# Kernel tuning notes

Hardware: AMD Instinct MI355X
Metric: run time of the kernel (lower is better)

Reference implementation:

```python
import jax, jax.numpy as jnp
import numpy as np

B, T, D = 16, 512, 256
HH = D // 2   # per-direction hidden of bidirectional GRU
G, Z, R, NA = 32, 8, 16, 18


def _gru_step(h, x, wih, whh, bih, bhh):
    # torch.nn.GRUCell math
    gi = x @ wih.T + bih
    gh = h @ whh.T + bhh
    ir, iz, inn = jnp.split(gi, 3, axis=-1)
    hr, hz, hn = jnp.split(gh, 3, axis=-1)
    r = jax.nn.sigmoid(ir + hr)
    z = jax.nn.sigmoid(iz + hz)
    n = jnp.tanh(inn + r * hn)
    return (1.0 - z) * n + z * h


def _gru_seq(x_tbd, wih, whh, bih, bhh):
    h0 = jnp.zeros((x_tbd.shape[1], whh.shape[1]), x_tbd.dtype)
    def step(h, x):
        h = _gru_step(h, x, wih, whh, bih, bhh)
        return h, h
    _, hs = jax.lax.scan(step, h0, x_tbd)
    return hs  # (T, B, H)


def setup_inputs() -> dict:
    key = jax.random.key(0)
    ks = jax.random.split(key, 26)
    rn = lambda k, s, sc: jax.random.normal(k, s, jnp.float32) * sc
    d = {
        'e_seq': rn(ks[0], (B, T, D), 1.0),
        'eps':   rn(ks[1], (B, T, Z), 1.0),
        # acausal bidirectional GRU (fwd + bwd cells)
        'wih_f': rn(ks[2], (3 * HH, D), D ** -0.5),  'whh_f': rn(ks[3], (3 * HH, HH), HH ** -0.5),
        'bih_f': jnp.zeros((3 * HH,)), 'bhh_f': jnp.zeros((3 * HH,)),
        'wih_b': rn(ks[4], (3 * HH, D), D ** -0.5),  'whh_b': rn(ks[5], (3 * HH, HH), HH ** -0.5),
        'bih_b': jnp.zeros((3 * HH,)), 'bhh_b': jnp.zeros((3 * HH,)),
        # controller encoder GRUCell(2D -> G) + heads
        'wih_e': rn(ks[6], (3 * G, 2 * D), (2 * D) ** -0.5), 'whh_e': rn(ks[7], (3 * G, G), G ** -0.5),
        'bih_e': jnp.zeros((3 * G,)), 'bhh_e': jnp.zeros((3 * G,)),
        'mu_w': rn(ks[8], (Z, G), G ** -0.5),  'mu_b': jnp.zeros((Z,)),
        'lv_w': rn(ks[9], (Z, G), G ** -0.5),  'lv_b': jnp.zeros((Z,)),
        # switching unit MLP (D+G+Z -> 64 -> 1)
        'sw1_w': rn(ks[10], (64, D + G + Z), (D + G + Z) ** -0.5), 'sw1_b': jnp.zeros((64,)),
        'sw2_w': rn(ks[11], (1, 64), 64 ** -0.5), 'sw2_b': jnp.zeros((1,)),
        # decoder hypernet (Z -> 32 -> 2*D*R)
        'dec1_w': rn(ks[12], (32, Z), Z ** -0.5), 'dec1_b': jnp.zeros((32,)),
        'dec2_w': rn(ks[13], (2 * D * R, 32), 32 ** -0.5), 'dec2_b': jnp.zeros((2 * D * R,)),
        # final norm + action head
        'ln_g': jnp.ones((D,)), 'ln_b': jnp.zeros((D,)),
        'head_w': rn(ks[14], (NA, D), D ** -0.5), 'head_b': jnp.zeros((NA,)),
    }
    return d


def _forward(e_seq, eps, wih_f, whh_f, bih_f, bhh_f, wih_b, whh_b, bih_b, bhh_b,
             wih_e, whh_e, bih_e, bhh_e, mu_w, mu_b, lv_w, lv_b,
             sw1_w, sw1_b, sw2_w, sw2_b, dec1_w, dec1_b, dec2_w, dec2_b,
             ln_g, ln_b, head_w, head_b):
    Bz, Tt, Dm = e_seq.shape
    e_tbd = jnp.swapaxes(e_seq, 0, 1)                      # (T, B, D)
    # AcausalEmbedder: bidirectional GRU
    fwd = _gru_seq(e_tbd, wih_f, whh_f, bih_f, bhh_f)
    bwd = _gru_seq(e_tbd[::-1], wih_b, whh_b, bih_b, bhh_b)[::-1]
    s_tbd = jnp.concatenate([fwd, bwd], axis=-1)           # (T, B, D)
    eps_tbd = jnp.swapaxes(eps, 0, 1)

    h0 = jnp.zeros((Bz, whh_e.shape[1]), e_seq.dtype)
    z0 = jnp.zeros((Bz, mu_w.shape[0]), e_seq.dtype)

    def step(carry, xs):
        h, z_prev = carry
        e_t, s_t, eps_t = xs
        h = _gru_step(h, jnp.concatenate([e_t, s_t], axis=-1), wih_e, whh_e, bih_e, bhh_e)
        mu = h @ mu_w.T + mu_b
        logvar = h @ lv_w.T + lv_b
        # switching unit uses updated h (causal)
        hid = jnp.tanh(jnp.concatenate([e_t, h, z_prev], axis=-1) @ sw1_w.T + sw1_b)
        beta = jax.nn.sigmoid(hid @ sw2_w.T + sw2_b)       # (B, 1)
        z = beta * (mu + jnp.exp(0.5 * logvar) * eps_t) + (1.0 - beta) * z_prev
        return (h, jax.lax.stop_gradient(z)), (mu, logvar, beta, z)

    _, (mu_t, lv_t, be_t, z_t) = jax.lax.scan(step, (h0, z0), (e_tbd, s_tbd, eps_tbd))
    mu_seq = jnp.swapaxes(mu_t, 0, 1)
    logvar_seq = jnp.swapaxes(lv_t, 0, 1)
    beta_seq = jnp.swapaxes(be_t, 0, 1)
    z_seq = jnp.swapaxes(z_t, 0, 1)                        # (B, T, Z)

    # ControllerDecoder: z -> (A, Bm); apply U = A @ Bm^T without materializing U
    hmid = jnp.tanh(z_seq @ dec1_w.T + dec1_b)
    ab = hmid @ dec2_w.T + dec2_b                          # (B, T, 2*D*R)
    DR = ab.shape[-1] // 2
    A = ab[..., :DR].reshape(Bz, Tt, Dm, -1)               # (B, T, D, R)
    Bm = ab[..., DR:].reshape(Bz, Tt, Dm, -1)
    tmp = jnp.einsum('btdr,btd->btr', Bm, e_seq)
    perturbed = e_seq + jnp.einsum('btdr,btr->btd', A, tmp)

    # final LayerNorm + action head on obs positions
    mean = perturbed.mean(-1, keepdims=True)
    var = perturbed.var(-1, keepdims=True)
    xn = (perturbed - mean) * jax.lax.rsqrt(var + 1e-5) * ln_g + ln_b
    logits = xn @ head_w.T + head_b                        # (B, T, NA)
    return logits, mu_seq, logvar_seq, beta_seq, z_seq


def reference(e_seq, eps, wih_f, whh_f, bih_f, bhh_f, wih_b, whh_b, bih_b, bhh_b,
              wih_e, whh_e, bih_e, bhh_e, mu_w, mu_b, lv_w, lv_b,
              sw1_w, sw1_b, sw2_w, sw2_b, dec1_w, dec1_b, dec2_w, dec2_b,
              ln_g, ln_b, head_w, head_b):
    return _forward(e_seq, eps, wih_f, whh_f, bih_f, bhh_f, wih_b, whh_b, bih_b, bhh_b,
                    wih_e, whh_e, bih_e, bhh_e, mu_w, mu_b, lv_w, lv_b,
                    sw1_w, sw1_b, sw2_w, sw2_b, dec1_w, dec1_b, dec2_w, dec2_b,
                    ln_g, ln_b, head_w, head_b)
```

## Files before the change

kernel.cpp:

```cpp
#include <hip/hip_runtime.h>

#define TT 512
#define BB 16
#define DD 256
#define HHH 128
#define GG 32
#define ZZ 8
#define RR_ 16
#define NAA 18

typedef _Float16 h2v __attribute__((ext_vector_type(2)));
typedef __attribute__((ext_vector_type(4))) float f4;
typedef __attribute__((ext_vector_type(4))) int i4;

__device__ __forceinline__ float sigmoid_(float x) { return 1.f / (1.f + __expf(-x)); }
__device__ __forceinline__ float tanh_(float x) { float e = __expf(2.f * x); return 1.f - 2.f / (e + 1.f); }
__device__ __forceinline__ float dot4(float4 a, float4 b) {
    return a.x * b.x + a.y * b.y + a.z * b.z + a.w * b.w;
}
__device__ __forceinline__ h2v u2h2(unsigned u) { union { unsigned u; h2v h; } c; c.u = u; return c.h; }

__device__ __forceinline__ void lds_barrier() {
    asm volatile("s_waitcnt lgkmcnt(0)" ::: "memory");
    __builtin_amdgcn_s_barrier();
}

template <int CTRL, int RM, int BM, bool BC>
__device__ __forceinline__ float dpp_add_f(float v) {
    return v + __int_as_float(__builtin_amdgcn_update_dpp(0, __float_as_int(v), CTRL, RM, BM, BC));
}
__device__ __forceinline__ float wave_sum_bcast(float p) {
    p = dpp_add_f<0x111, 0xf, 0xf, true>(p);
    p = dpp_add_f<0x112, 0xf, 0xf, true>(p);
    p = dpp_add_f<0x114, 0xf, 0xf, true>(p);
    p = dpp_add_f<0x118, 0xf, 0xf, true>(p);
    p = dpp_add_f<0x142, 0xa, 0xf, false>(p);
    p = dpp_add_f<0x143, 0xc, 0xf, false>(p);
    return __int_as_float(__builtin_amdgcn_readlane(__float_as_int(p), 63));
}
__device__ __forceinline__ float quad_sum(float v) {
    v = dpp_add_f<0xB1, 0xf, 0xf, true>(v);
    v = dpp_add_f<0x4E, 0xf, 0xf, true>(v);
    return v;
}
__device__ __forceinline__ float rdlane(float v, int l) {
    return __int_as_float(__builtin_amdgcn_readlane(__float_as_int(v), l));
}

__global__ __launch_bounds__(256) void pack_w(
    const float* __restrict__ wf, const float* __restrict__ wb,
    const float* __restrict__ we,
    unsigned* __restrict__ pk, unsigned* __restrict__ pk_e)
{
    int i = blockIdx.x * 256 + threadIdx.x;
    if (i < 49152) {
        int dir = i / 24576; int r = i % 24576;
        int w = r / 3072;    int r2 = r % 3072;
        int T = r2 / 1024;   int r3 = r2 % 1024;
        int kt = r3 / 256;   int r4 = r3 % 256;
        int lane = r4 / 4;   int jd = r4 % 4;
        const float* wsrc = dir ? wb : wf;
        int row = T * 128 + 16 * w + (lane & 15);
        int k0 = kt * 32 + (lane >> 4) * 8 + 2 * jd;
        union { _Float16 h[2]; unsigned u; } c;
        c.h[0] = (_Float16)wsrc[row * 128 + k0];
        c.h[1] = (_Float16)wsrc[row * 128 + k0 + 1];
        pk[i] = c.u;
    } else if (i < 50688) {
        int ie = i - 49152;
        int s = ie / 384;  int rem = ie % 384;
        int k = rem / 12;  int e = rem % 12;
        int j = e / 4;     int m = e % 4;
        int row = j * 32 + k, k0 = 8 * s + 2 * m;
        union { _Float16 h[2]; unsigned u; } c;
        c.h[0] = (_Float16)we[row * 32 + k0];
        c.h[1] = (_Float16)we[row * 32 + k0 + 1];
        pk_e[ie] = c.u;
    }
}

__global__ __launch_bounds__(256) void gemm_k(
    const float* __restrict__ A, int K, const float* __restrict__ W, int ldw,
    const float* __restrict__ bias, float* __restrict__ Out, int ldout, int N, int accFlag)
{
    __shared__ float At[64][36];
    __shared__ float Wt[32][36];
    int row0 = blockIdx.x * 64, n0 = blockIdx.y * 32;
    int tid = threadIdx.x;
    int tx = tid & 15, ty = tid >> 4;
    float acc[4][2] = {};
    for (int k0 = 0; k0 < K; k0 += 32) {
        #pragma unroll
        for (int i = 0; i < 8; ++i) {
            int idx = tid + i * 256; int rr = idx >> 5, kk = idx & 31;
            At[rr][kk] = A[(size_t)(row0 + rr) * K + k0 + kk];
        }
        #pragma unroll
        for (int i = 0; i < 4; ++i) {
            int idx = tid + i * 256; int nn = idx >> 5, kk = idx & 31;
            Wt[nn][kk] = (n0 + nn < N) ? W[(size_t)(n0 + nn) * ldw + k0 + kk] : 0.f;
        }
        __syncthreads();
        #pragma unroll
        for (int kk = 0; kk < 32; kk += 4) {
            float4 w0 = *(const float4*)&Wt[tx][kk];
            float4 w1 = *(const float4*)&Wt[tx + 16][kk];
            #pragma unroll
            for (int rr = 0; rr < 4; ++rr) {
                float4 av = *(const float4*)&At[ty * 4 + rr][kk];
                acc[rr][0] += dot4(av, w0);
                acc[rr][1] += dot4(av, w1);
            }
        }
        __syncthreads();
    }
    #pragma unroll
    for (int cc = 0; cc < 2; ++cc) {
        int n = n0 + tx + cc * 16;
        if (n < N) {
            float badd = bias ? bias[n] : 0.f;
            #pragma unroll
            for (int rr = 0; rr < 4; ++rr) {
                int row = row0 + ty * 4 + rr;
                float v = acc[rr][cc] + badd;
                if (accFlag) Out[(size_t)row * ldout + n] += v;
                else         Out[(size_t)row * ldout + n] = v;
            }
        }
    }
}

__global__ __launch_bounds__(256) void gemm_gi(
    const float* __restrict__ A,
    const float* __restrict__ wf, const float* __restrict__ bf, float* __restrict__ of,
    const float* __restrict__ wb, const float* __restrict__ bb, float* __restrict__ ob)
{
    __shared__ float At[64][36];
    __shared__ float Wt[32][36];
    int y = blockIdx.y;
    const float* W; const float* bias; float* Out; int n0;
    if (y < 12) { W = wf; bias = bf; Out = of; n0 = y * 32; }
    else        { W = wb; bias = bb; Out = ob; n0 = (y - 12) * 32; }
    int row0 = blockIdx.x * 64;
    int tid = threadIdx.x;
    int tx = tid & 15, ty = tid >> 4;
    float acc[4][2] = {};
    for (int k0 = 0; k0 < 256; k0 += 32) {
        #pragma unroll
        for (int i = 0; i < 8; ++i) {
            int idx = tid + i * 256; int rr = idx >> 5, kk = idx & 31;
            At[rr][kk] = A[(size_t)(row0 + rr) * 256 + k0 + kk];
        }
        #pragma unroll
        for (int i = 0; i < 4; ++i) {
            int idx = tid + i * 256; int nn = idx >> 5, kk = idx & 31;
            Wt[nn][kk] = W[(size_t)(n0 + nn) * 256 + k0 + kk];
        }
        __syncthreads();
        #pragma unroll
        for (int kk = 0; kk < 32; kk += 4) {
            float4 w0 = *(const float4*)&Wt[tx][kk];
            float4 w1 = *(const float4*)&Wt[tx + 16][kk];
            #pragma unroll
            for (int rr = 0; rr < 4; ++rr) {
                float4 av = *(const float4*)&At[ty * 4 + rr][kk];
                acc[rr][0] += dot4(av, w0);
                acc[rr][1] += dot4(av, w1);
            }
        }
        __syncthreads();
    }
    #pragma unroll
    for (int cc = 0; cc < 2; ++cc) {
        int n = n0 + tx + cc * 16;
        float badd = bias[n];
        #pragma unroll
        for (int rr = 0; rr < 4; ++rr) {
            int row = row0 + ty * 4 + rr;
            Out[(size_t)row * 384 + n] = acc[rr][cc] + badd;
        }
    }
}

struct __align__(16) SmGru { _Float16 hb[2][128]; };
struct __align__(16) SmGemm { float At[64][36]; float Wt[32][36]; };
union __align__(16) SmU { SmGru g; SmGemm m; };

__device__ __forceinline__ void gemm_tile256(
    const float* __restrict__ A, int K, const float* __restrict__ W, int ldw,
    const float* __restrict__ bias, float* __restrict__ Out, int ldout, int N,
    int row0, int n0, SmGemm& sm)
{
    int tid = threadIdx.x;
    int tx = tid & 15, ty = tid >> 4;
    float acc[4][2] = {};
    for (int k0 = 0; k0 < K; k0 += 32) {
        #pragma unroll
        for (int i = 0; i < 8; ++i) {
            int idx = tid + i * 256; int rr = idx >> 5, kk = idx & 31;
            sm.At[rr][kk] = A[(size_t)(row0 + rr) * K + k0 + kk];
        }
        #pragma unroll
        for (int i = 0; i < 4; ++i) {
            int idx = tid + i * 256; int nn = idx >> 5, kk = idx & 31;
            sm.Wt[nn][kk] = (n0 + nn < N) ? W[(size_t)(n0 + nn) * ldw + k0 + kk] : 0.f;
        }
        __syncthreads();
        #pragma unroll
        for (int kk = 0; kk < 32; kk += 4) {
            float4 w0 = *(const float4*)&sm.Wt[tx][kk];
            float4 w1 = *(const float4*)&sm.Wt[tx + 16][kk];
            #pragma unroll
            for (int rr = 0; rr < 4; ++rr) {
                float4 av = *(const float4*)&sm.At[ty * 4 + rr][kk];
                acc[rr][0] += dot4(av, w0);
                acc[rr][1] += dot4(av, w1);
            }
        }
        __syncthreads();
    }
    #pragma unroll
    for (int cc = 0; cc < 2; ++cc) {
        int n = n0 + tx + cc * 16;
        if (n < N) {
            float badd = bias[n];
            #pragma unroll
            for (int rr = 0; rr < 4; ++rr)
                Out[(size_t)(row0 + ty * 4 + rr) * ldout + n] = acc[rr][cc] + badd;
        }
    }
}

__global__ __launch_bounds__(256, 2) void gru_fused(
    const float* __restrict__ gi_f, const float* __restrict__ gi_b,
    const unsigned* __restrict__ pk,
    const float* __restrict__ bhh_f, const float* __restrict__ bhh_b,
    float* __restrict__ s_seq,
    const float* __restrict__ e,
    const float* __restrict__ wih_e, const float* __restrict__ bih_e, float* __restrict__ gie,
    const float* __restrict__ sw1_w, const float* __restrict__ sw1_b, float* __restrict__ swe)
{
    __shared__ SmU sm;
    int bx = blockIdx.x;
    if (bx >= 416) {
        int t = bx - 416;
        gemm_tile256(e, 256, sw1_w, 296, sw1_b, swe, 64, 64, (t & 127) * 64, (t >> 7) * 32, sm.m);
        return;
    }
    if (bx >= 32) {
        int t = bx - 32;
        gemm_tile256(e, 256, wih_e, 512, bih_e, gie, 96, 96, (t & 127) * 64, (t >> 7) * 32, sm.m);
        return;
    }

    int dir = bx >> 4, b = bx & 15;
    const float* gi  = dir ? gi_b  : gi_f;
    const float* bhh = dir ? bhh_b : bhh_f;
    int tid = threadIdx.x;
    int w = tid >> 6;
    int lane = tid & 63;
    int quad = lane >> 4;
    int j = 32 * w + (lane & 31);

    i4 bf[2][3][4];
    #pragma unroll
    for (int tt = 0; tt < 2; ++tt)
        #pragma unroll
        for (int T = 0; T < 3; ++T)
            #pragma unroll
            for (int kt = 0; kt < 4; ++kt)
                bf[tt][T][kt] = *(const i4*)(pk + (size_t)((((dir * 8 + 2 * w + tt) * 3 + T) * 4 + kt) * 64 + lane) * 4);
    #pragma unroll
    for (int tt = 0; tt < 2; ++tt)
        #pragma unroll
        for (int T = 0; T < 3; ++T)
            #pragma unroll
            for (int kt = 0; kt < 4; ++kt)
                asm volatile("" : "+a"(bf[tt][T][kt]));

    if (tid < 128) sm.g.hb[0][tid] = (_Float16)0.f;

    float bhr = 0.f, bhz = 0.f, bhn = 0.f;
    float gra = 0.f, gza = 0.f, gna = 0.f;
    float grb = 0.f, gzb = 0.f, gnb = 0.f;
    float hreg = 0.f;
    if (lane < 32) {
        bhr = bhh[j]; bhz = bhh[128 + j]; bhn = bhh[256 + j];
        int t0 = dir ? 511 : 0;
        int t1 = dir ? 510 : 1;
        size_t p0 = (size_t)(b * TT + t0) * 384;
        size_t p1 = (size_t)(b * TT + t1) * 384;
        gra = gi[p0 + j]; gza = gi[p0 + 128 + j]; gna = gi[p0 + 256 + j];
        grb = gi[p1 + j]; gzb = gi[p1 + 128 + j]; gnb = gi[p1 + 256 + j];
    }
    __syncthreads();

    int cur = 0;
    auto body = [&](int step, float& gr, float& gz, float& gn) {
        i4 af[4];
        #pragma unroll
        for (int kt = 0; kt < 4; ++kt)
            af[kt] = *(const i4*)(&sm.g.hb[cur][kt * 32 + quad * 8]);
        f4 accr0 = {0.f, 0.f, 0.f, 0.f}, accr1 = {0.f, 0.f, 0.f, 0.f};
        f4 accz0 = {0.f, 0.f, 0.f, 0.f}, accz1 = {0.f, 0.f, 0.f, 0.f};
        f4 accn0 = {0.f, 0.f, 0.f, 0.f}, accn1 = {0.f, 0.f, 0.f, 0.f};
        asm volatile("s_nop 3" : "+v"(accr0), "+v"(accz0), "+v"(accn0),
                                 "+v"(accr1), "+v"(accz1), "+v"(accn1));
        #pragma unroll
        for (int kt = 0; kt < 4; ++kt) {
            asm volatile("v_mfma_f32_16x16x32_f16 %0, %1, %2, %0" : "+v"(accr0) : "v"(af[kt]), "a"(bf[0][0][kt]));
            asm volatile("v_mfma_f32_16x16x32_f16 %0, %1, %2, %0" : "+v"(accz0) : "v"(af[kt]), "a"(bf[0][1][kt]));
            asm volatile("v_mfma_f32_16x16x32_f16 %0, %1, %2, %0" : "+v"(accn0) : "v"(af[kt]), "a"(bf[0][2][kt]));
            asm volatile("v_mfma_f32_16x16x32_f16 %0, %1, %2, %0" : "+v"(accr1) : "v"(af[kt]), "a"(bf[1][0][kt]));
            asm volatile("v_mfma_f32_16x16x32_f16 %0, %1, %2, %0" : "+v"(accz1) : "v"(af[kt]), "a"(bf[1][1][kt]));
            asm volatile("v_mfma_f32_16x16x32_f16 %0, %1, %2, %0" : "+v"(accn1) : "v"(af[kt]), "a"(bf[1][2][kt]));
        }
        asm volatile("s_nop 7\n\ts_nop 7" : "+v"(accr0), "+v"(accz0), "+v"(accn0),
                                            "+v"(accr1), "+v"(accz1), "+v"(accn1));
        if (lane < 32) {
            int t = dir ? (511 - step) : step;
            int p = b * TT + t;
            bool hi = lane >= 16;
            float ar = hi ? accr1[0] : accr0[0];
            float az = hi ? accz1[0] : accz0[0];
            float an = hi ? accn1[0] : accn0[0];
            float r = sigmoid_(gr + bhr + ar);
            float z = sigmoid_(gz + bhz + az);
            float n = tanh_(gn + r * (bhn + an));
            float hn = (1.f - z) * n + z * hreg;
            hreg = hn;
            sm.g.hb[cur ^ 1][j] = (_Float16)hn;
            s_seq[(size_t)p * 256 + dir * 128 + j] = hn;
            int s2 = step + 2;
            int tp = (s2 < 512) ? (dir ? (511 - s2) : s2) : t;
            size_t p2 = (size_t)(b * TT + tp) * 384;
            gr = gi[p2 + j]; gz = gi[p2 + 128 + j]; gn = gi[p2 + 256 + j];
        }
        lds_barrier();
        cur ^= 1;
    };

    for (int step = 0; step < 512; step += 2) {
        body(step,     gra, gza, gna);
        body(step + 1, grb, gzb, gnb);
    }
}

__global__ __launch_bounds__(128, 1) void ctrl_fused(
    const float* __restrict__ gie, const unsigned* __restrict__ pk_e,
    const float* __restrict__ bhh_e,
    const float* __restrict__ mu_w, const float* __restrict__ mu_b,
    const float* __restrict__ lv_w, const float* __restrict__ lv_b,
    const float* __restrict__ sw1_w, const float* __restrict__ sw2_w,
    const float* __restrict__ sw2_b,
    const float* __restrict__ swe,
    const float* __restrict__ eps,
    float* __restrict__ out_mu, float* __restrict__ out_lv,
    float* __restrict__ beta_o, float* __restrict__ z_o)
{
    int b = blockIdx.x;
    int tid = threadIdx.x;
    int wid = tid >> 6;
    int lane = tid & 63;
    int pbase = b * TT;

    __shared__ __align__(16) _Float16 hb[32][32];
    __shared__ __align__(16) float    hf[32][32];

    int k = lane >> 1, s2 = lane & 1;
    unsigned wg[24];
    float bhr = 0.f, bhz = 0.f, bhn = 0.f, hreg = 0.f;
    float g1[16] = {}, g2[16] = {}, g3[16] = {};
    if (wid == 0) {
        #pragma unroll
        for (int ss = 0; ss < 2; ++ss) {
            const uint4* wp = (const uint4*)(pk_e + ((size_t)((2 * s2 + ss) * 32) + k) * 12);
            #pragma unroll
            for (int i = 0; i < 3; ++i) {
                uint4 u = wp[i];
                wg[12 * ss + 4 * i + 0] = u.x;
                wg[12 * ss + 4 * i + 1] = u.y;
                wg[12 * ss + 4 * i + 2] = u.z;
                wg[12 * ss + 4 * i + 3] = u.w;
            }
        }
        if (lane < 32) hb[31][lane] = (_Float16)0.f;
        if (s2 == 0) {
            bhr = bhh_e[k]; bhz = bhh_e[32 + k]; bhn = bhh_e[64 + k];
            #pragma unroll
            for (int i = 0; i < 16; ++i) {
                size_t p = (size_t)(pbase + i) * 96;
                g1[i] = gie[p + k]; g2[i] = gie[p + 32 + k]; g3[i] = gie[p + 64 + k];
            }
        }
    }

    int x = lane >> 3, kind = (lane >> 2) & 1, s = lane & 3;
    float4 swh4[8];
    float4 wz0v = {0,0,0,0}, wz1v = {0,0,0,0}, mlw0 = {0,0,0,0}, mlw1 = {0,0,0,0};
    float w2 = 0.f, sb2 = 0.f, mlb = 0.f;
    float4 zr0 = {0.f, 0.f, 0.f, 0.f}, zr1 = {0.f, 0.f, 0.f, 0.f};
    float hp[16] = {}, ep[16] = {};
    if (wid == 1) {
        #pragma unroll
        for (int i = 0; i < 8; ++i)
            swh4[i] = *(const float4*)(sw1_w + (size_t)lane * 296 + 256 + 4 * i);
        wz0v = *(const float4*)(sw1_w + (size_t)lane * 296 + 288);
        wz1v = *(const float4*)(sw1_w + (size_t)lane * 296 + 292);
        w2 = sw2_w[lane];
        sb2 = sw2_b[0];
        const float* mw = kind ? lv_w : mu_w;
        mlw0 = *(const float4*)(mw + x * 32 + 8 * s);
        mlw1 = *(const float4*)(mw + x * 32 + 8 * s + 4);
        mlb = kind ? lv_b[x] : mu_b[x];
        #pragma unroll
        for (int i = 0; i < 16; ++i) {
            hp[i] = swe[(size_t)(pbase + i) * 64 + lane];
            ep[i] = eps[(size_t)(pbase + i) * 8 + x];
        }
    }
    __syncthreads();

    auto prod_step = [&](int t, float& ga, float& gb, float& gc) {
        const uint4* hv = (const uint4*)(&hb[(t - 1) & 31][16 * s2]);
        uint4 hA = hv[0], hB = hv[1];
        unsigned hw[8] = {hA.x, hA.y, hA.z, hA.w, hB.x, hB.y, hB.z, hB.w};
        float a0 = 0.f, a1 = 0.f, a2 = 0.f, c0 = 0.f, c1 = 0.f, c2 = 0.f;
        #pragma unroll
        for (int m = 0; m < 4; ++m) {
            a0 = __builtin_amdgcn_fdot2(u2h2(wg[m]),      u2h2(hw[m]),     a0, false);
            a1 = __builtin_amdgcn_fdot2(u2h2(wg[4 + m]),  u2h2(hw[m]),     a1, false);
            a2 = __builtin_amdgcn_fdot2(u2h2(wg[8 + m]),  u2h2(hw[m]),     a2, false);
            c0 = __builtin_amdgcn_fdot2(u2h2(wg[12 + m]), u2h2(hw[4 + m]), c0, false);
            c1 = __builtin_amdgcn_fdot2(u2h2(wg[16 + m]), u2h2(hw[4 + m]), c1, false);
            c2 = __builtin_amdgcn_fdot2(u2h2(wg[20 + m]), u2h2(hw[4 + m]), c2, false);
        }
        a0 += c0; a1 += c1; a2 += c2;
        a0 = dpp_add_f<0xB1, 0xf, 0xf, true>(a0);
        a1 = dpp_add_f<0xB1, 0xf, 0xf, true>(a1);
        a2 = dpp_add_f<0xB1, 0xf, 0xf, true>(a2);
        if (s2 == 0) {
            float r = sigmoid_(ga + bhr + a0);
            float z = sigmoid_(gb + bhz + a1);
            float n = tanh_(gc + r * (bhn + a2));
            float hn = (1.f - z) * n + z * hreg;
            hreg = hn;
            hb[t & 31][k] = (_Float16)hn;
            hf[t & 31][k] = hn;
            int t16 = (t + 16 < 512) ? (t + 16) : t;
            size_t p2 = (size_t)(pbase + t16) * 96;
            ga = gie[p2 + k]; gb = gie[p2 + 32 + k]; gc = gie[p2 + 64 + k];
        }
    };

    auto cons_step = [&](int t, float& hpi, float& epi) {
        int sl = t & 31;
        const float4* hv4 = (const float4*)(&hf[sl][0]);
        float4 h0 = hv4[0], h1 = hv4[1], h2 = hv4[2], h3 = hv4[3];
        float4 h4 = hv4[4], h5 = hv4[5], h6 = hv4[6], h7 = hv4[7];
        float d0 = dot4(swh4[0], h0) + dot4(swh4[1], h1);
        float d1 = dot4(swh4[2], h2) + dot4(swh4[3], h3);
        float d2 = dot4(swh4[4], h4) + dot4(swh4[5], h5);
        float d3 = dot4(swh4[6], h6) + dot4(swh4[7], h7);
        float hsum = (d0 + d1) + (d2 + d3);
        float4 hs0 = *(const float4*)(&hf[sl][8 * s]);
        float4 hs1 = *(const float4*)(&hf[sl][8 * s + 4]);
        float pacc = quad_sum(dot4(mlw0, hs0) + dot4(mlw1, hs1));
        float v = pacc + mlb;
        float other = __int_as_float(__builtin_amdgcn_ds_swizzle(__float_as_int(v), 0x101F));
        float muv = kind ? other : v;
        float lvv = kind ? v : other;
        float cand = muv + __expf(0.5f * lvv) * epi;
        float sc0 = rdlane(cand, 0),  sc1 = rdlane(cand, 8);
        float sc2 = rdlane(cand, 16), sc3 = rdlane(cand, 24);
        float sc4 = rdlane(cand, 32), sc5 = rdlane(cand, 40);
        float sc6 = rdlane(cand, 48), sc7 = rdlane(cand, 56);
        float az = dot4(wz0v, zr0) + dot4(wz1v, zr1);
        float a = (hpi + hsum) + az;
        float hid = tanh_(a);
        float beta = sigmoid_(wave_sum_bcast(w2 * hid) + sb2);
        float omb = 1.f - beta;
        zr0.x = beta * sc0 + omb * zr0.x; zr0.y = beta * sc1 + omb * zr0.y;
        zr0.z = beta * sc2 + omb * zr0.z; zr0.w = beta * sc3 + omb * zr0.w;
        zr1.x = beta * sc4 + omb * zr1.x; zr1.y = beta * sc5 + omb * zr1.y;
        zr1.z = beta * sc6 + omb * zr1.z; zr1.w = beta * sc7 + omb * zr1.w;
        int p = pbase + t;
        if (lane == 0) {
            beta_o[p] = beta;
            *(float4*)(z_o + (size_t)p * 8)     = zr0;
            *(float4*)(z_o + (size_t)p * 8 + 4) = zr1;
        }
        if ((lane & 7) == 0) out_mu[(size_t)p * 8 + x] = muv;
        if ((lane & 7) == 4) out_lv[(size_t)p * 8 + x] = lvv;
        int t16 = (t + 16 < 512) ? (t + 16) : t;
        hpi = swe[(size_t)(pbase + t16) * 64 + lane];
        epi = eps[(size_t)(pbase + t16) * 8 + x];
    };

    for (int ph = 0; ph < 33; ++ph) {
        if (wid == 0) {
            if (ph < 32) {
                int t0 = ph * 16;
                #pragma unroll
                for (int i = 0; i < 16; ++i)
                    prod_step(t0 + i, g1[i], g2[i], g3[i]);
            }
        } else {
            if (ph >= 1) {
                int t0 = (ph - 1) * 16;
                #pragma unroll
                for (int i = 0; i < 16; ++i)
                    cons_step(t0 + i, hp[i], ep[i]);
            }
        }
        lds_barrier();
    }
}

__global__ __launch_bounds__(256, 3) void decoder_final(
    const float* __restrict__ e_seq, const float* __restrict__ z_o,
    const float* __restrict__ dec1_w, const float* __restrict__ dec1_b,
    const float* __restrict__ dec2_w, const float* __restrict__ dec2_b,
    const float* __restrict__ ln_g, const float* __restrict__ ln_b,
    const float* __restrict__ head_w, const float* __restrict__ head_b,
    float* __restrict__ logits)
{
    __shared__ __align__(16) float e_l[8][256];
    __shared__ __align__(16) float hmid[8][32];
    __shared__ float zl[8][8];
    __shared__ float tmpw[8][16];
    __shared__ __align__(16) float partb[2048];
    __shared__ float red1[8][16];
    __shared__ float red2[8][16];
    __shared__ float stats[8][2];
    int tid = threadIdx.x;
    int p0 = blockIdx.x * 8;

    {
        const float4* eg = (const float4*)(e_seq + (size_t)p0 * 256);
        float4* el4 = (float4*)&e_l[0][0];
        el4[tid] = eg[tid];
        el4[tid + 256] = eg[tid + 256];
        if (tid < 64) ((float*)zl)[tid] = z_o[p0 * 8 + tid];
    }
    __syncthreads();
    {
        int pp = tid >> 5, g = tid & 31;
        float a = dec1_b[g];
        #pragma unroll
        for (int x = 0; x < 8; ++x) a += dec1_w[g * 8 + x] * zl[pp][x];
        hmid[pp][g] = tanh_(a);
    }
    __syncthreads();
    {
        int r = tid & 15, dgrp = tid >> 4;
        float acc[8];
        #pragma unroll
        for (int pp = 0; pp < 8; ++pp) acc[pp] = 0.f;
        for (int iblk = 0; iblk < 8; ++iblk) {
            float4 wr[2][8]; float wb[2]; int dd[2];
            #pragma unroll
            for (int ii = 0; ii < 2; ++ii) {
                int d = dgrp + 16 * (iblk * 2 + ii);
                dd[ii] = d;
                int row = 4096 + d * 16 + r;
                const float4* wp = (const float4*)(dec2_w + (size_t)row * 32);
                #pragma unroll
                for (int g = 0; g < 8; ++g) wr[ii][g] = wp[g];
                wb[ii] = dec2_b[row];
            }
            #pragma unroll 1
            for (int pp = 0; pp < 8; ++pp) {
                const float4* hv = (const float4*)hmid[pp];
                float b0 = wb[0], b1 = wb[1];
                #pragma unroll
                for (int g = 0; g < 8; ++g) {
                    float4 hh = hv[g];
                    b0 += dot4(wr[0][g], hh);
                    b1 += dot4(wr[1][g], hh);
                }
                acc[pp] += b0 * e_l[pp][dd[0]] + b1 * e_l[pp][dd[1]];
            }
        }
        #pragma unroll
        for (int pp = 0; pp < 8; ++pp) partb[(pp * 16 + r) * 16 + dgrp] = acc[pp];
    }
    __syncthreads();
    if (tid < 128) {
        int pp = tid >> 4, rr = tid & 15;
        float s = 0.f;
        #pragma unroll
        for (int dg = 0; dg < 16; ++dg) s += partb[(pp * 16 + rr) * 16 + dg];
        tmpw[pp][rr] = s;
    }
    __syncthreads();
    {
        int d = tid;
        float po[8];
        #pragma unroll
        for (int pp = 0; pp < 8; ++pp) po[pp] = e_l[pp][d];
        for (int rblk = 0; rblk < 8; ++rblk) {
            float4 wr[2][8]; float wb[2];
            #pragma unroll
            for (int ii = 0; ii < 2; ++ii) {
                int row = d * 16 + rblk * 2 + ii;
                const float4* wp = (const float4*)(dec2_w + (size_t)row * 32);
                #pragma unroll
                for (int g = 0; g < 8; ++g) wr[ii][g] = wp[g];
                wb[ii] = dec2_b[row];
            }
            #pragma unroll 1
            for (int pp = 0; pp < 8; ++pp) {
                const float4* hv = (const float4*)hmid[pp];
                float a0 = wb[0], a1 = wb[1];
                #pragma unroll
                for (int g = 0; g < 8; ++g) {
                    float4 hh = hv[g];
                    a0 += dot4(wr[0][g], hh);
                    a1 += dot4(wr[1][g], hh);
                }
                po[pp] += a0 * tmpw[pp][rblk * 2] + a1 * tmpw[pp][rblk * 2 + 1];
            }
        }
        #pragma unroll
        for (int pp = 0; pp < 8; ++pp) partb[pp * 256 + d] = po[pp];
    }
    __syncthreads();
    if (tid < 128) {
        int pp = tid >> 4, c = tid & 15;
        float s = 0.f, s2 = 0.f;
        #pragma unroll
        for (int i = 0; i < 16; ++i) { float v = partb[pp * 256 + c * 16 + i]; s += v; s2 += v * v; }
        red1[pp][c] = s; red2[pp][c] = s2;
    }
    __syncthreads();
    if (tid < 8) {
        float s = 0.f, s2 = 0.f;
        #pragma unroll
        for (int c = 0; c < 16; ++c) { s += red1[tid][c]; s2 += red2[tid][c]; }
        float mean = s * (1.f / 256.f);
        float var = s2 * (1.f / 256.f) - mean * mean;
        stats[tid][0] = mean;
        stats[tid][1] = rsqrtf(var + 1e-5f);
    }
    __syncthreads();
    {
        int d = tid;
        float g = ln_g[d], bln = ln_b[d];
        #pragma unroll
        for (int pp = 0; pp < 8; ++pp) {
            float v = (partb[pp * 256 + d] - stats[pp][0]) * stats[pp][1];
            partb[pp * 256 + d] = v * g + bln;
        }
    }
    __syncthreads();
    if (tid < 144) {
        int pp = tid / 18, na = tid - pp * 18;
        float a = head_b[na];
        for (int d2 = 0; d2 < 256; ++d2)
            a += partb[pp * 256 + d2] * head_w[na * 256 + d2];
        logits[(size_t)(p0 + pp) * 18 + na] = a;
    }
}

extern "C" void kernel_launch(void* const* d_in, const int* in_sizes, int n_in,
                              void* d_out, int out_size, void* d_ws, size_t ws_size,
                              hipStream_t stream) {
    (void)in_sizes; (void)n_in; (void)out_size; (void)ws_size;
    const float* e     = (const float*)d_in[0];
    const float* eps   = (const float*)d_in[1];
    const float* wih_f = (const float*)d_in[2];
    const float* whh_f = (const float*)d_in[3];
    const float* bih_f = (const float*)d_in[4];
    const float* bhh_f = (const float*)d_in[5];
    const float* wih_b = (const float*)d_in[6];
    const float* whh_b = (const float*)d_in[7];
    const float* bih_b = (const float*)d_in[8];
    const float* bhh_b = (const float*)d_in[9];
    const float* wih_e = (const float*)d_in[10];
    const float* whh_e = (const float*)d_in[11];
    const float* bih_e = (const float*)d_in[12];
    const float* bhh_e = (const float*)d_in[13];
    const float* mu_w  = (const float*)d_in[14];
    const float* mu_b  = (const float*)d_in[15];
    const float* lv_w  = (const float*)d_in[16];
    const float* lv_b  = (const float*)d_in[17];
    const float* sw1_w = (const float*)d_in[18];
    const float* sw1_b = (const float*)d_in[19];
    const float* sw2_w = (const float*)d_in[20];
    const float* sw2_b = (const float*)d_in[21];
    const float* dec1_w = (const float*)d_in[22];
    const float* dec1_b = (const float*)d_in[23];
    const float* dec2_w = (const float*)d_in[24];
    const float* dec2_b = (const float*)d_in[25];
    const float* ln_g  = (const float*)d_in[26];
    const float* ln_b  = (const float*)d_in[27];
    const float* head_w = (const float*)d_in[28];
    const float* head_b = (const float*)d_in[29];

    float* ws    = (float*)d_ws;
    float* gi_f  = ws;
    float* gi_b  = gi_f + 3145728;
    float* gie   = gi_b + 3145728;
    float* swe   = gie + 786432;
    float* s_seq = swe + 524288;
    float* h_seq = s_seq + 2097152;
    unsigned* pk   = (unsigned*)(h_seq + 262144);
    unsigned* pk_e = pk + 49152;
    (void)h_seq;

    float* out       = (float*)d_out;
    float* out_logit = out;
    float* out_mu    = out + 147456;
    float* out_lv    = out + 212992;
    float* out_beta  = out + 278528;
    float* out_z     = out + 286720;

    pack_w<<<198, 256, 0, stream>>>(whh_f, whh_b, whh_e, pk, pk_e);
    gemm_gi<<<dim3(128, 24), 256, 0, stream>>>(e, wih_f, bih_f, gi_f, wih_b, bih_b, gi_b);
    gru_fused<<<672, 256, 0, stream>>>(gi_f, gi_b, pk, bhh_f, bhh_b, s_seq,
                                       e, wih_e, bih_e, gie, sw1_w, sw1_b, swe);
    gemm_k<<<dim3(128, 3), 256, 0, stream>>>(s_seq, 256, wih_e + 256, 512, nullptr, gie, 96, 96, 1);
    ctrl_fused<<<16, 128, 0, stream>>>(gie, pk_e, bhh_e, mu_w, mu_b, lv_w, lv_b,
                                       sw1_w, sw2_w, sw2_b, swe, eps,
                                       out_mu, out_lv, out_beta, out_z);
    decoder_final<<<1024, 256, 0, stream>>>(e, out_z, dec1_w, dec1_b, dec2_w, dec2_b,
                                            ln_g, ln_b, head_w, head_b, out_logit);
}
```

Measured before the change: 888.6 us.

## Interleave two batch sequences per controller block to hide recurrence latency

The controller recurrence kernel now processes two batch elements per block, interleaving their independent GRU and switching steps so each wave has two dependency chains to overlap. The grid halves from 16 to 8 blocks and the phase length shrinks from 16 to 8 steps, with ring buffers and prefetch depth adjusted to match. This aims to hide the serial latency of each step by issuing independent work between dependent operations. In exchange, the work per block doubles, and register pressure from the duplicated state could reduce the benefit.

```diff
diff --git a/kernel.cpp b/kernel.cpp
--- a/kernel.cpp
+++ b/kernel.cpp
@@ -358,19 +358,22 @@
     float* __restrict__ out_mu, float* __restrict__ out_lv,
     float* __restrict__ beta_o, float* __restrict__ z_o)
 {
-    int b = blockIdx.x;
+    int bx = blockIdx.x;
     int tid = threadIdx.x;
     int wid = tid >> 6;
     int lane = tid & 63;
-    int pbase = b * TT;
-
-    __shared__ __align__(16) _Float16 hb[32][32];
-    __shared__ __align__(16) float    hf[32][32];
+    int pb0 = (2 * bx) * TT;
+    int pb1 = (2 * bx + 1) * TT;
+
+    __shared__ __align__(16) _Float16 hb[2][16][32];
+    __shared__ __align__(16) float    hf[2][16][32];
 
     int k = lane >> 1, s2 = lane & 1;
     unsigned wg[24];
-    float bhr = 0.f, bhz = 0.f, bhn = 0.f, hreg = 0.f;
-    float g1[16] = {}, g2[16] = {}, g3[16] = {};
+    float bhr = 0.f, bhz = 0.f, bhn = 0.f;
+    float hreg0 = 0.f, hreg1 = 0.f;
+    float g1a[8] = {}, g2a[8] = {}, g3a[8] = {};
+    float g1b[8] = {}, g2b[8] = {}, g3b[8] = {};
     if (wid == 0) {
         #pragma unroll
         for (int ss = 0; ss < 2; ++ss) {
@@ -384,13 +387,15 @@
                 wg[12 * ss + 4 * i + 3] = u.w;
             }
         }
-        if (lane < 32) hb[31][lane] = (_Float16)0.f;
+        if (lane < 32) { hb[0][15][lane] = (_Float16)0.f; hb[1][15][lane] = (_Float16)0.f; }
         if (s2 == 0) {
             bhr = bhh_e[k]; bhz = bhh_e[32 + k]; bhn = bhh_e[64 + k];
             #pragma unroll
-            for (int i = 0; i < 16; ++i) {
-                size_t p = (size_t)(pbase + i) * 96;
-                g1[i] = gie[p + k]; g2[i] = gie[p + 32 + k]; g3[i] = gie[p + 64 + k];
+            for (int i = 0; i < 8; ++i) {
+                size_t pa = (size_t)(pb0 + i) * 96;
+                size_t pbq = (size_t)(pb1 + i) * 96;
+                g1a[i] = gie[pa + k];  g2a[i] = gie[pa + 32 + k];  g3a[i] = gie[pa + 64 + k];
+                g1b[i] = gie[pbq + k]; g2b[i] = gie[pbq + 32 + k]; g3b[i] = gie[pbq + 64 + k];
             }
         }
     }
@@ -399,8 +404,8 @@
     float4 swh4[8];
     float4 wz0v = {0,0,0,0}, wz1v = {0,0,0,0}, mlw0 = {0,0,0,0}, mlw1 = {0,0,0,0};
     float w2 = 0.f, sb2 = 0.f, mlb = 0.f;
-    float4 zr0 = {0.f, 0.f, 0.f, 0.f}, zr1 = {0.f, 0.f, 0.f, 0.f};
-    float hp[16] = {}, ep[16] = {};
+    float4 zr0a = {0,0,0,0}, zr1a = {0,0,0,0}, zr0b = {0,0,0,0}, zr1b = {0,0,0,0};
+    float hpa[8] = {}, epa[8] = {}, hpb[8] = {}, epb[8] = {};
     if (wid == 1) {
         #pragma unroll
         for (int i = 0; i < 8; ++i)
@@ -414,15 +419,19 @@
         mlw1 = *(const float4*)(mw + x * 32 + 8 * s + 4);
         mlb = kind ? lv_b[x] : mu_b[x];
         #pragma unroll
-        for (int i = 0; i < 16; ++i) {
-            hp[i] = swe[(size_t)(pbase + i) * 64 + lane];
-            ep[i] = eps[(size_t)(pbase + i) * 8 + x];
-        }
-    }
-    __syncthreads();
-
-    auto prod_step = [&](int t, float& ga, float& gb, float& gc) {
-        const uint4* hv = (const uint4*)(&hb[(t - 1) & 31][16 * s2]);
+        for (int i = 0; i < 8; ++i) {
+            hpa[i] = swe[(size_t)(pb0 + i) * 64 + lane];
+            epa[i] = eps[(size_t)(pb0 + i) * 8 + x];
+            hpb[i] = swe[(size_t)(pb1 + i) * 64 + lane];
+            epb[i] = eps[(size_t)(pb1 + i) * 8 + x];
+        }
+    }
+    __syncthreads();
+
+    auto prod_step = [&](int t, int pbase, float& hr,
+                         float& ga, float& gb, float& gc,
+                         _Float16 (*hbB)[32], float (*hfB)[32]) {
+        const uint4* hv = (const uint4*)(&hbB[(t - 1) & 15][16 * s2]);
         uint4 hA = hv[0], hB = hv[1];
         unsigned hw[8] = {hA.x, hA.y, hA.z, hA.w, hB.x, hB.y, hB.z, hB.w};
         float a0 = 0.f, a1 = 0.f, a2 = 0.f, c0 = 0.f, c1 = 0.f, c2 = 0.f;
@@ -443,19 +452,20 @@
             float r = sigmoid_(ga + bhr + a0);
             float z = sigmoid_(gb + bhz + a1);
             float n = tanh_(gc + r * (bhn + a2));
-            float hn = (1.f - z) * n + z * hreg;
-            hreg = hn;
-            hb[t & 31][k] = (_Float16)hn;
-            hf[t & 31][k] = hn;
-            int t16 = (t + 16 < 512) ? (t + 16) : t;
-            size_t p2 = (size_t)(pbase + t16) * 96;
+            float hn = (1.f - z) * n + z * hr;
+            hr = hn;
+            hbB[t & 15][k] = (_Float16)hn;
+            hfB[t & 15][k] = hn;
+            int t8 = (t + 8 < 512) ? (t + 8) : t;
+            size_t p2 = (size_t)(pbase + t8) * 96;
             ga = gie[p2 + k]; gb = gie[p2 + 32 + k]; gc = gie[p2 + 64 + k];
         }
     };
 
-    auto cons_step = [&](int t, float& hpi, float& epi) {
-        int sl = t & 31;
-        const float4* hv4 = (const float4*)(&hf[sl][0]);
+    auto cons_step = [&](int t, int pbase, float4& z0, float4& z1,
+                         float& hpi, float& epi, float (*hfB)[32]) {
+        int sl = t & 15;
+        const float4* hv4 = (const float4*)(&hfB[sl][0]);
         float4 h0 = hv4[0], h1 = hv4[1], h2 = hv4[2], h3 = hv4[3];
         float4 h4 = hv4[4], h5 = hv4[5], h6 = hv4[6], h7 = hv4[7];
         float d0 = dot4(swh4[0], h0) + dot4(swh4[1], h1);
@@ -463,8 +473,8 @@
         float d2 = dot4(swh4[4], h4) + dot4(swh4[5], h5);
         float d3 = dot4(swh4[6], h6) + dot4(swh4[7], h7);
         float hsum = (d0 + d1) + (d2 + d3);
-        float4 hs0 = *(const float4*)(&hf[sl][8 * s]);
-        float4 hs1 = *(const float4*)(&hf[sl][8 * s + 4]);
+        float4 hs0 = *(const float4*)(&hfB[sl][8 * s]);
+        float4 hs1 = *(const float4*)(&hfB[sl][8 * s + 4]);
         float pacc = quad_sum(dot4(mlw0, hs0) + dot4(mlw1, hs1));
         float v = pacc + mlb;
         float other = __int_as_float(__builtin_amdgcn_ds_swizzle(__float_as_int(v), 0x101F));
@@ -475,42 +485,46 @@
         float sc2 = rdlane(cand, 16), sc3 = rdlane(cand, 24);
         float sc4 = rdlane(cand, 32), sc5 = rdlane(cand, 40);
         float sc6 = rdlane(cand, 48), sc7 = rdlane(cand, 56);
-        float az = dot4(wz0v, zr0) + dot4(wz1v, zr1);
+        float az = dot4(wz0v, z0) + dot4(wz1v, z1);
         float a = (hpi + hsum) + az;
         float hid = tanh_(a);
         float beta = sigmoid_(wave_sum_bcast(w2 * hid) + sb2);
         float omb = 1.f - beta;
-        zr0.x = beta * sc0 + omb * zr0.x; zr0.y = beta * sc1 + omb * zr0.y;
-        zr0.z = beta * sc2 + omb * zr0.z; zr0.w = beta * sc3 + omb * zr0.w;
-        zr1.x = beta * sc4 + omb * zr1.x; zr1.y = beta * sc5 + omb * zr1.y;
-        zr1.z = beta * sc6 + omb * zr1.z; zr1.w = beta * sc7 + omb * zr1.w;
+        z0.x = beta * sc0 + omb * z0.x; z0.y = beta * sc1 + omb * z0.y;
+        z0.z = beta * sc2 + omb * z0.z; z0.w = beta * sc3 + omb * z0.w;
+        z1.x = beta * sc4 + omb * z1.x; z1.y = beta * sc5 + omb * z1.y;
+        z1.z = beta * sc6 + omb * z1.z; z1.w = beta * sc7 + omb * z1.w;
         int p = pbase + t;
         if (lane == 0) {
             beta_o[p] = beta;
-            *(float4*)(z_o + (size_t)p * 8)     = zr0;
-            *(float4*)(z_o + (size_t)p * 8 + 4) = zr1;
+            *(float4*)(z_o + (size_t)p * 8)     = z0;
+            *(float4*)(z_o + (size_t)p * 8 + 4) = z1;
         }
         if ((lane & 7) == 0) out_mu[(size_t)p * 8 + x] = muv;
         if ((lane & 7) == 4) out_lv[(size_t)p * 8 + x] = lvv;
-        int t16 = (t + 16 < 512) ? (t + 16) : t;
-        hpi = swe[(size_t)(pbase + t16) * 64 + lane];
-        epi = eps[(size_t)(pbase + t16) * 8 + x];
+        int t8 = (t + 8 < 512) ? (t + 8) : t;
+        hpi = swe[(size_t)(pbase + t8) * 64 + lane];
+        epi = eps[(size_t)(pbase + t8) * 8 + x];
     };
 
-    for (int ph = 0; ph < 33; ++ph) {
+    for (int ph = 0; ph < 65; ++ph) {
         if (wid == 0) {
-            if (ph < 32) {
-                int t0 = ph * 16;
+            if (ph < 64) {
+                int t0 = ph * 8;
                 #pragma unroll
-                for (int i = 0; i < 16; ++i)
-                    prod_step(t0 + i, g1[i], g2[i], g3[i]);
+                for (int i = 0; i < 8; ++i) {
+                    prod_step(t0 + i, pb0, hreg0, g1a[i], g2a[i], g3a[i], hb[0], hf[0]);
+                    prod_step(t0 + i, pb1, hreg1, g1b[i], g2b[i], g3b[i], hb[1], hf[1]);
+                }
             }
         } else {
             if (ph >= 1) {
-                int t0 = (ph - 1) * 16;
+                int t0 = (ph - 1) * 8;
                 #pragma unroll
-                for (int i = 0; i < 16; ++i)
-                    cons_step(t0 + i, hp[i], ep[i]);
+                for (int i = 0; i < 8; ++i) {
+                    cons_step(t0 + i, pb0, zr0a, zr1a, hpa[i], epa[i], hf[0]);
+                    cons_step(t0 + i, pb1, zr0b, zr1b, hpb[i], epb[i], hf[1]);
+                }
             }
         }
         lds_barrier();
@@ -721,9 +735,9 @@
     gru_fused<<<672, 256, 0, stream>>>(gi_f, gi_b, pk, bhh_f, bhh_b, s_seq,
                                        e, wih_e, bih_e, gie, sw1_w, sw1_b, swe);
     gemm_k<<<dim3(128, 3), 256, 0, stream>>>(s_seq, 256, wih_e + 256, 512, nullptr, gie, 96, 96, 1);
-    ctrl_fused<<<16, 128, 0, stream>>>(gie, pk_e, bhh_e, mu_w, mu_b, lv_w, lv_b,
-                                       sw1_w, sw2_w, sw2_b, swe, eps,
-                                       out_mu, out_lv, out_beta, out_z);
+    ctrl_fused<<<8, 128, 0, stream>>>(gie, pk_e, bhh_e, mu_w, mu_b, lv_w, lv_b,
+                                      sw1_w, sw2_w, sw2_b, swe, eps,
+                                      out_mu, out_lv, out_beta, out_z);
     decoder_final<<<1024, 256, 0, stream>>>(e, out_z, dec1_w, dec1_b, dec2_w, dec2_b,
                                             ln_g, ln_b, head_w, head_b, out_logit);
 }
```

Measured after the change: 1.129 ms. 1.27x slower.
